# Performance work log

Measured on AMD Instinct MI355X. Metric: run time of the kernel, lower is better.

Reference implementation:

```python
import jax, jax.numpy as jnp
import numpy as np

N = 100000
E = 3200000
F_IN = 256
HID = 128


def _dconv_k1(x_cat, w, b):
    # torch_geometric_temporal DConv with K=1:
    # H = X @ W[0,0] + X @ W[1,0] + b   (no graph propagation for K=1)
    return x_cat @ (w[0, 0] + w[1, 0]) + b


def _dcrnn_cell(x, h, wz, bz, wr, br, wh, bh):
    xh = jnp.concatenate([x, h], axis=1)
    z = jax.nn.sigmoid(_dconv_k1(xh, wz, bz))
    r = jax.nn.sigmoid(_dconv_k1(xh, wr, br))
    xrh = jnp.concatenate([x, r * h], axis=1)
    h_tilde = jnp.tanh(_dconv_k1(xrh, wh, bh))
    return z * h + (1.0 - z) * h_tilde


def setup_inputs() -> dict:
    key = jax.random.key(0)
    ks = jax.random.split(key, 16)

    def gw(k, shape):
        fan_in = shape[-2]
        return jax.random.normal(k, shape, dtype=jnp.float32) / np.sqrt(fan_in)

    inp = {
        "x": jax.random.normal(ks[0], (N, F_IN), dtype=jnp.float32),
        "edge_index": jax.random.randint(ks[1], (2, E), 0, N, dtype=jnp.int64 if jax.config.jax_enable_x64 else jnp.int32),
        "edge_weight": jax.random.uniform(ks[2], (E,), dtype=jnp.float32),
        "w_z1": gw(ks[3], (2, 1, F_IN + HID, HID)), "b_z1": jnp.zeros((HID,), jnp.float32),
        "w_r1": gw(ks[4], (2, 1, F_IN + HID, HID)), "b_r1": jnp.zeros((HID,), jnp.float32),
        "w_h1": gw(ks[5], (2, 1, F_IN + HID, HID)), "b_h1": jnp.zeros((HID,), jnp.float32),
        "w_z2": gw(ks[6], (2, 1, HID + HID // 2, HID // 2)), "b_z2": jnp.zeros((HID // 2,), jnp.float32),
        "w_r2": gw(ks[7], (2, 1, HID + HID // 2, HID // 2)), "b_r2": jnp.zeros((HID // 2,), jnp.float32),
        "w_h2": gw(ks[8], (2, 1, HID + HID // 2, HID // 2)), "b_h2": jnp.zeros((HID // 2,), jnp.float32),
        "w_lin1": gw(ks[9], (HID // 2, 16)), "b_lin1": jnp.zeros((16,), jnp.float32),
        "w_lin2": gw(ks[10], (16, 1)), "b_lin2": jnp.zeros((1,), jnp.float32),
    }
    return inp


def reference(x, edge_index, edge_weight,
              w_z1, b_z1, w_r1, b_r1, w_h1, b_h1,
              w_z2, b_z2, w_r2, b_r2, w_h2, b_h2,
              w_lin1, b_lin1, w_lin2, b_lin2):
    # edge_index / edge_weight are unused in the K=1 DConv math (faithful to tgt source).
    h0 = jnp.zeros((x.shape[0], w_z1.shape[-1]), x.dtype)
    h = _dcrnn_cell(x, h0, w_z1, b_z1, w_r1, b_r1, w_h1, b_h1)
    h = jax.nn.relu(h)
    h0b = jnp.zeros((x.shape[0], w_z2.shape[-1]), x.dtype)
    h = _dcrnn_cell(h, h0b, w_z2, b_z2, w_r2, b_r2, w_h2, b_h2)
    h = jax.nn.relu(h)
    # Dropout(0.2) is identity at inference
    h = jax.nn.relu(h @ w_lin1 + b_lin1)
    return h @ w_lin2 + b_lin2
```

## Files before the change

### kernel.cpp

```cpp
#include <hip/hip_runtime.h>

typedef _Float16 f16;
typedef _Float16 f16x4 __attribute__((ext_vector_type(4)));
typedef _Float16 f16x8 __attribute__((ext_vector_type(8)));
typedef float    f32x4 __attribute__((ext_vector_type(4)));

#define N_ROWS 100000
#define RT 782
#define TPB 512
#define LSX 264
#define LSH1 136
#define LSH2 72

#define W1F_OFF 0
#define W1F_BYTES (256 * 256 * 2)
#define W2F_OFF W1F_BYTES

#define ARENA 67584
#define H1S 0
#define H2S 34816

__global__ void prep_w(const float* __restrict__ wz1, const float* __restrict__ wh1,
                       const float* __restrict__ wz2, const float* __restrict__ wh2,
                       f16* __restrict__ W1F, f16* __restrict__ W2F) {
    const int b = blockIdx.x, tid = threadIdx.x;
    if (b < 32) {
        int idx = b * 256 + tid;
        int l = idx & 63, itm = idx >> 6;
        int it = itm & 7, M = itm >> 3;
        int ln = l & 15, q = l >> 4;
        int col = M * 16 + ln;
        int k0 = it * 32 + q * 8;
        const float* w = (col < 128) ? wz1 : wh1;
        int cc = col & 127;
        f16x8 v;
#pragma unroll
        for (int j = 0; j < 8; ++j) {
            int k = k0 + j;
            v[j] = (f16)(w[k * 128 + cc] + w[384 * 128 + k * 128 + cc]);
        }
        *(f16x8*)&W1F[idx * 8] = v;
    } else {
        int idx = (b - 32) * 256 + tid;
        if (idx >= 2048) return;
        int l = idx & 63, tkc = idx >> 6;
        int kc = tkc & 3, t = tkc >> 2;
        int ln = l & 15, q = l >> 4;
        int col = (t < 4) ? (16 * t + ln) : (64 + 16 * (t - 4) + ln);
        int k0 = kc * 32 + q * 8;
        const float* w = (col < 64) ? wz2 : wh2;
        int cc = col & 63;
        f16x8 v;
#pragma unroll
        for (int j = 0; j < 8; ++j) {
            int k = k0 + j;
            v[j] = (f16)(w[k * 64 + cc] + w[192 * 64 + k * 64 + cc]);
        }
        *(f16x8*)&W2F[idx * 8] = v;
    }
}

__device__ __forceinline__ float gate(float zp, float hp) {
    float e2h = __expf(2.0f * fminf(hp, 15.0f));
    float ez  = __expf(zp);
    float r   = __builtin_amdgcn_rcpf((e2h + 1.0f) * (1.0f + ez));
    return fmaxf((e2h - 1.0f) * r, 0.0f);
}

__global__ __launch_bounds__(TPB, 4) void fused(
    const float* __restrict__ x,
    const f16* __restrict__ W1F, const f16* __restrict__ W2F,
    const float* __restrict__ bz1, const float* __restrict__ bh1,
    const float* __restrict__ bz2, const float* __restrict__ bh2,
    const float* __restrict__ wl1, const float* __restrict__ bl1,
    const float* __restrict__ wl2, const float* __restrict__ bl2,
    float* __restrict__ out)
{
    __shared__ __align__(16) char arena[ARENA];
    const int tid = threadIdx.x, lane = tid & 63, wave = tid >> 6;
    const int ln = lane & 15, quad = lane >> 4;
    const int r0 = blockIdx.x * 128;

    const int xr = tid >> 2, xcg = tid & 3;
    int gxr = r0 + xr; if (gxr >= N_ROWS) gxr = N_ROWS - 1;
    const float* xp = x + (size_t)gxr * 256 + (xcg << 3);

    f16* Xs = (f16*)arena;

    const f16* wbz = W1F + ((size_t)(wave * 8) * 64 + lane) * 8;
    const f16* wbh = W1F + ((size_t)((wave + 8) * 8) * 64 + lane) * 8;

    f32x4 acc[2][8];
#pragma unroll
    for (int a = 0; a < 2; ++a)
#pragma unroll
        for (int b = 0; b < 8; ++b) acc[a][b] = (f32x4){0.f, 0.f, 0.f, 0.f};

    f32x4 pa = __builtin_nontemporal_load((const f32x4*)(xp));
    f32x4 pb = __builtin_nontemporal_load((const f32x4*)(xp + 4));
    f16x8 afz = *(const f16x8*)(wbz);
    f16x8 afh = *(const f16x8*)(wbh);

#pragma unroll
    for (int s = 0; s < 8; ++s) {
        *(f16x8*)&Xs[xr * LSX + s * 32 + (xcg << 3)] =
            (f16x8){(f16)pa[0],(f16)pa[1],(f16)pa[2],(f16)pa[3],
                    (f16)pb[0],(f16)pb[1],(f16)pb[2],(f16)pb[3]};
        __syncthreads();
        f16x8 afz_n, afh_n;
        if (s < 7) {
            pa = __builtin_nontemporal_load((const f32x4*)(xp + (s + 1) * 32));
            pb = __builtin_nontemporal_load((const f32x4*)(xp + (s + 1) * 32 + 4));
            afz_n = *(const f16x8*)(wbz + (s + 1) * 512);
            afh_n = *(const f16x8*)(wbh + (s + 1) * 512);
        }
        __builtin_amdgcn_sched_barrier(0);
#pragma unroll
        for (int nt = 0; nt < 8; ++nt) {
            f16x8 bf = *(const f16x8*)&Xs[(16 * nt + ln) * LSX + s * 32 + quad * 8];
            acc[0][nt] = __builtin_amdgcn_mfma_f32_16x16x32_f16(afz, bf, acc[0][nt], 0, 0, 0);
            acc[1][nt] = __builtin_amdgcn_mfma_f32_16x16x32_f16(afh, bf, acc[1][nt], 0, 0, 0);
        }
        afz = afz_n; afh = afh_n;
    }
    __syncthreads();

    const int c = wave & 3, rh = wave >> 2;
    f16x8 w2f[2][4];
#pragma unroll
    for (int kc = 0; kc < 4; ++kc) {
        w2f[0][kc] = *(const f16x8*)(W2F + ((size_t)((c    ) * 4 + kc) * 64 + lane) * 8);
        w2f[1][kc] = *(const f16x8*)(W2F + ((size_t)((c + 4) * 4 + kc) * 64 + lane) * 8);
    }

    f16* h1s = (f16*)(arena + H1S);
    {
        const int jg0 = 16 * wave + (quad << 2);
        const float4 zb = *(const float4*)(bz1 + jg0);
        const float4 hb = *(const float4*)(bh1 + jg0);
#pragma unroll
        for (int nt = 0; nt < 8; ++nt) {
            const int row = 16 * nt + ln;
            f16x4 pk;
#pragma unroll
            for (int i = 0; i < 4; ++i)
                pk[i] = (f16)gate(acc[0][nt][i] + (&zb.x)[i],
                                  acc[1][nt][i] + (&hb.x)[i]);
            *(f16x4*)&h1s[row * LSH1 + jg0] = pk;
        }
    }
    __syncthreads();

    f32x4 acc2[2][4];
#pragma unroll
    for (int a = 0; a < 2; ++a)
#pragma unroll
        for (int b = 0; b < 4; ++b) acc2[a][b] = (f32x4){0.f, 0.f, 0.f, 0.f};
#pragma unroll
    for (int kc = 0; kc < 4; ++kc) {
        f16x8 bf[4];
#pragma unroll
        for (int nt = 0; nt < 4; ++nt)
            bf[nt] = *(const f16x8*)&h1s[(16 * (4 * rh + nt) + ln) * LSH1 + kc * 32 + quad * 8];
#pragma unroll
        for (int m = 0; m < 2; ++m)
#pragma unroll
            for (int nt = 0; nt < 4; ++nt)
                acc2[m][nt] = __builtin_amdgcn_mfma_f32_16x16x32_f16(w2f[m][kc], bf[nt], acc2[m][nt], 0, 0, 0);
    }

    f16* h2s = (f16*)(arena + H2S);
    {
        const int jg0 = 16 * c + (quad << 2);
        const float4 zb = *(const float4*)(bz2 + jg0);
        const float4 hb = *(const float4*)(bh2 + jg0);
#pragma unroll
        for (int nt = 0; nt < 4; ++nt) {
            const int row = 16 * (4 * rh + nt) + ln;
            f16x4 pk;
#pragma unroll
            for (int i = 0; i < 4; ++i)
                pk[i] = (f16)gate(acc2[0][nt][i] + (&zb.x)[i],
                                  acc2[1][nt][i] + (&hb.x)[i]);
            *(f16x4*)&h2s[row * LSH2 + jg0] = pk;
        }
    }
    __syncthreads();

    const float blv = bl1[ln], wlv = wl2[ln], bl2v = bl2[0];
    f16x8 bfr[2];
#pragma unroll
    for (int kc = 0; kc < 2; ++kc)
#pragma unroll
        for (int j = 0; j < 8; ++j)
            bfr[kc][j] = (f16)wl1[(32 * kc + 8 * quad + j) * 16 + ln];

    f32x4 acc3 = (f32x4){0.f, 0.f, 0.f, 0.f};
#pragma unroll
    for (int kc = 0; kc < 2; ++kc) {
        f16x8 af = *(const f16x8*)&h2s[(16 * wave + ln) * LSH2 + kc * 32 + quad * 8];
        acc3 = __builtin_amdgcn_mfma_f32_16x16x32_f16(af, bfr[kc], acc3, 0, 0, 0);
    }
#pragma unroll
    for (int i = 0; i < 4; ++i) {
        float v = fmaxf(acc3[i] + blv, 0.0f) * wlv;
        v += __shfl_xor(v, 1);
        v += __shfl_xor(v, 2);
        v += __shfl_xor(v, 4);
        v += __shfl_xor(v, 8);
        if (ln == 0) {
            const int row = r0 + 16 * wave + (quad << 2) + i;
            if (row < N_ROWS) out[row] = v + bl2v;
        }
    }
}

extern "C" void kernel_launch(void* const* d_in, const int* in_sizes, int n_in,
                              void* d_out, int out_size, void* d_ws, size_t ws_size,
                              hipStream_t stream) {
    const float* x   = (const float*)d_in[0];
    const float* wz1 = (const float*)d_in[3];
    const float* bz1 = (const float*)d_in[4];
    const float* wh1 = (const float*)d_in[7];
    const float* bh1 = (const float*)d_in[8];
    const float* wz2 = (const float*)d_in[9];
    const float* bz2 = (const float*)d_in[10];
    const float* wh2 = (const float*)d_in[13];
    const float* bh2 = (const float*)d_in[14];
    const float* wl1 = (const float*)d_in[15];
    const float* bl1 = (const float*)d_in[16];
    const float* wl2 = (const float*)d_in[17];
    const float* bl2 = (const float*)d_in[18];

    char* ws = (char*)d_ws;
    f16* W1F = (f16*)(ws + W1F_OFF);
    f16* W2F = (f16*)(ws + W2F_OFF);
    float* out = (float*)d_out;

    prep_w<<<40, 256, 0, stream>>>(wz1, wh1, wz2, wh2, W1F, W2F);
    fused<<<RT, TPB, 0, stream>>>(x, W1F, W2F, bz1, bh1, bz2, bh2,
                                  wl1, bl1, wl2, bl2, out);
}
```

Baseline: 219.2 us.

## Halve block to 64 rows with 4 waves, each computing 4 output tiles

Shrinks each block from 128 rows and 8 waves to 64 rows and 4 waves, doubling the grid and halving LDS use. Each wave now owns four weight M-tiles (two z, two h) across four row tiles instead of two M-tiles across eight. The layer-2 and output stages are remapped to the 4-wave layout. This aims for more resident blocks and better latency hiding, at the cost of re-reading the layer-1 weights twice as often per row and dropping the weight-fragment prefetch.

New measurement: 221.1 us. About the same (+0.9%).

```diff
diff --git a/kernel.cpp b/kernel.cpp
--- a/kernel.cpp
+++ b/kernel.cpp
@@ -6,8 +6,8 @@
 typedef float    f32x4 __attribute__((ext_vector_type(4)));
 
 #define N_ROWS 100000
-#define RT 782
-#define TPB 512
+#define RT 1563
+#define TPB 256
 #define LSX 264
 #define LSH1 136
 #define LSH2 72
@@ -16,9 +16,9 @@
 #define W1F_BYTES (256 * 256 * 2)
 #define W2F_OFF W1F_BYTES
 
-#define ARENA 67584
+#define ARENA 33792
 #define H1S 0
-#define H2S 34816
+#define H2S 17408
 
 __global__ void prep_w(const float* __restrict__ wz1, const float* __restrict__ wh1,
                        const float* __restrict__ wz2, const float* __restrict__ wh2,
@@ -79,7 +79,7 @@
     __shared__ __align__(16) char arena[ARENA];
     const int tid = threadIdx.x, lane = tid & 63, wave = tid >> 6;
     const int ln = lane & 15, quad = lane >> 4;
-    const int r0 = blockIdx.x * 128;
+    const int r0 = blockIdx.x * 64;
 
     const int xr = tid >> 2, xcg = tid & 3;
     int gxr = r0 + xr; if (gxr >= N_ROWS) gxr = N_ROWS - 1;
@@ -87,19 +87,16 @@
 
     f16* Xs = (f16*)arena;
 
-    const f16* wbz = W1F + ((size_t)(wave * 8) * 64 + lane) * 8;
-    const f16* wbh = W1F + ((size_t)((wave + 8) * 8) * 64 + lane) * 8;
-
-    f32x4 acc[2][8];
-#pragma unroll
-    for (int a = 0; a < 2; ++a)
-#pragma unroll
-        for (int b = 0; b < 8; ++b) acc[a][b] = (f32x4){0.f, 0.f, 0.f, 0.f};
+    const f16* wb0 = W1F + (size_t)wave * 4096 + (size_t)lane * 8;
+
+    f32x4 acc[4][4];
+#pragma unroll
+    for (int a = 0; a < 4; ++a)
+#pragma unroll
+        for (int b = 0; b < 4; ++b) acc[a][b] = (f32x4){0.f, 0.f, 0.f, 0.f};
 
     f32x4 pa = __builtin_nontemporal_load((const f32x4*)(xp));
     f32x4 pb = __builtin_nontemporal_load((const f32x4*)(xp + 4));
-    f16x8 afz = *(const f16x8*)(wbz);
-    f16x8 afh = *(const f16x8*)(wbh);
 
 #pragma unroll
     for (int s = 0; s < 8; ++s) {
@@ -107,76 +104,77 @@
             (f16x8){(f16)pa[0],(f16)pa[1],(f16)pa[2],(f16)pa[3],
                     (f16)pb[0],(f16)pb[1],(f16)pb[2],(f16)pb[3]};
         __syncthreads();
-        f16x8 afz_n, afh_n;
         if (s < 7) {
             pa = __builtin_nontemporal_load((const f32x4*)(xp + (s + 1) * 32));
             pb = __builtin_nontemporal_load((const f32x4*)(xp + (s + 1) * 32 + 4));
-            afz_n = *(const f16x8*)(wbz + (s + 1) * 512);
-            afh_n = *(const f16x8*)(wbh + (s + 1) * 512);
-        }
+        }
+        f16x8 af[4];
+#pragma unroll
+        for (int mi = 0; mi < 4; ++mi)
+            af[mi] = *(const f16x8*)(wb0 + mi * 16384 + s * 512);
         __builtin_amdgcn_sched_barrier(0);
 #pragma unroll
-        for (int nt = 0; nt < 8; ++nt) {
+        for (int nt = 0; nt < 4; ++nt) {
             f16x8 bf = *(const f16x8*)&Xs[(16 * nt + ln) * LSX + s * 32 + quad * 8];
-            acc[0][nt] = __builtin_amdgcn_mfma_f32_16x16x32_f16(afz, bf, acc[0][nt], 0, 0, 0);
-            acc[1][nt] = __builtin_amdgcn_mfma_f32_16x16x32_f16(afh, bf, acc[1][nt], 0, 0, 0);
-        }
-        afz = afz_n; afh = afh_n;
+#pragma unroll
+            for (int mi = 0; mi < 4; ++mi)
+                acc[mi][nt] = __builtin_amdgcn_mfma_f32_16x16x32_f16(af[mi], bf, acc[mi][nt], 0, 0, 0);
+        }
     }
     __syncthreads();
 
-    const int c = wave & 3, rh = wave >> 2;
     f16x8 w2f[2][4];
 #pragma unroll
     for (int kc = 0; kc < 4; ++kc) {
-        w2f[0][kc] = *(const f16x8*)(W2F + ((size_t)((c    ) * 4 + kc) * 64 + lane) * 8);
-        w2f[1][kc] = *(const f16x8*)(W2F + ((size_t)((c + 4) * 4 + kc) * 64 + lane) * 8);
+        w2f[0][kc] = *(const f16x8*)(W2F + ((size_t)((wave    ) * 4 + kc) * 64 + lane) * 8);
+        w2f[1][kc] = *(const f16x8*)(W2F + ((size_t)((wave + 4) * 4 + kc) * 64 + lane) * 8);
     }
 
     f16* h1s = (f16*)(arena + H1S);
+#pragma unroll
+    for (int zi = 0; zi < 2; ++zi) {
+        const int jg0 = 16 * (wave + 4 * zi) + (quad << 2);
+        const float4 zb = *(const float4*)(bz1 + jg0);
+        const float4 hb = *(const float4*)(bh1 + jg0);
+#pragma unroll
+        for (int nt = 0; nt < 4; ++nt) {
+            const int row = 16 * nt + ln;
+            f16x4 pk;
+#pragma unroll
+            for (int i = 0; i < 4; ++i)
+                pk[i] = (f16)gate(acc[zi][nt][i] + (&zb.x)[i],
+                                  acc[zi + 2][nt][i] + (&hb.x)[i]);
+            *(f16x4*)&h1s[row * LSH1 + jg0] = pk;
+        }
+    }
+    __syncthreads();
+
+    f32x4 acc2[2][4];
+#pragma unroll
+    for (int a = 0; a < 2; ++a)
+#pragma unroll
+        for (int b = 0; b < 4; ++b) acc2[a][b] = (f32x4){0.f, 0.f, 0.f, 0.f};
+#pragma unroll
+    for (int kc = 0; kc < 4; ++kc) {
+        f16x8 bf[4];
+#pragma unroll
+        for (int nt = 0; nt < 4; ++nt)
+            bf[nt] = *(const f16x8*)&h1s[(16 * nt + ln) * LSH1 + kc * 32 + quad * 8];
+#pragma unroll
+        for (int m = 0; m < 2; ++m)
+#pragma unroll
+            for (int nt = 0; nt < 4; ++nt)
+                acc2[m][nt] = __builtin_amdgcn_mfma_f32_16x16x32_f16(w2f[m][kc], bf[nt], acc2[m][nt], 0, 0, 0);
+    }
+
+    f16* h2s = (f16*)(arena + H2S);
     {
         const int jg0 = 16 * wave + (quad << 2);
-        const float4 zb = *(const float4*)(bz1 + jg0);
-        const float4 hb = *(const float4*)(bh1 + jg0);
-#pragma unroll
-        for (int nt = 0; nt < 8; ++nt) {
-            const int row = 16 * nt + ln;
-            f16x4 pk;
-#pragma unroll
-            for (int i = 0; i < 4; ++i)
-                pk[i] = (f16)gate(acc[0][nt][i] + (&zb.x)[i],
-                                  acc[1][nt][i] + (&hb.x)[i]);
-            *(f16x4*)&h1s[row * LSH1 + jg0] = pk;
-        }
-    }
-    __syncthreads();
-
-    f32x4 acc2[2][4];
-#pragma unroll
-    for (int a = 0; a < 2; ++a)
-#pragma unroll
-        for (int b = 0; b < 4; ++b) acc2[a][b] = (f32x4){0.f, 0.f, 0.f, 0.f};
-#pragma unroll
-    for (int kc = 0; kc < 4; ++kc) {
-        f16x8 bf[4];
-#pragma unroll
-        for (int nt = 0; nt < 4; ++nt)
-            bf[nt] = *(const f16x8*)&h1s[(16 * (4 * rh + nt) + ln) * LSH1 + kc * 32 + quad * 8];
-#pragma unroll
-        for (int m = 0; m < 2; ++m)
-#pragma unroll
-            for (int nt = 0; nt < 4; ++nt)
-                acc2[m][nt] = __builtin_amdgcn_mfma_f32_16x16x32_f16(w2f[m][kc], bf[nt], acc2[m][nt], 0, 0, 0);
-    }
-
-    f16* h2s = (f16*)(arena + H2S);
-    {
-        const int jg0 = 16 * c + (quad << 2);
         const float4 zb = *(const float4*)(bz2 + jg0);
         const float4 hb = *(const float4*)(bh2 + jg0);
 #pragma unroll
         for (int nt = 0; nt < 4; ++nt) {
-            const int row = 16 * (4 * rh + nt) + ln;
+            const int row = 16 * nt + ln;
             f16x4 pk;
 #pragma unroll
             for (int i = 0; i < 4; ++i)
```
